# Optimization experiments

Measured on AMD Instinct MI355X. Metric: run time of the kernel, lower is better.

## Reference

```python
import jax, jax.numpy as jnp
import numpy as np

EMBED = 1024
HEADS = 16
HEAD_SIZE = EMBED // HEADS
B, T = 2, 2048
EPS = 1e-5


def layer_norm(x, g, b):
    mu = jnp.mean(x, axis=-1, keepdims=True)
    var = jnp.var(x, axis=-1, keepdims=True)
    return (x - mu) * jax.lax.rsqrt(var + EPS) * g + b


def setup_inputs() -> dict:
    key = jax.random.key(0)
    ks = jax.random.split(key, 12)
    s = 0.02
    return {
        "x": jax.random.normal(ks[0], (B, T, EMBED), jnp.float32),
        "Wq": s * jax.random.normal(ks[1], (EMBED, EMBED), jnp.float32),
        "Wk": s * jax.random.normal(ks[2], (EMBED, EMBED), jnp.float32),
        "Wv": s * jax.random.normal(ks[3], (EMBED, EMBED), jnp.float32),
        "Wo": s * jax.random.normal(ks[4], (EMBED, EMBED), jnp.float32),
        "bo": jnp.zeros((EMBED,), jnp.float32),
        "W1": s * jax.random.normal(ks[5], (EMBED, 4 * EMBED), jnp.float32),
        "b1": jnp.zeros((4 * EMBED,), jnp.float32),
        "W2": s * jax.random.normal(ks[6], (4 * EMBED, EMBED), jnp.float32),
        "b2": jnp.zeros((EMBED,), jnp.float32),
        "ln1_g": jnp.ones((EMBED,), jnp.float32),
        "ln1_b": jnp.zeros((EMBED,), jnp.float32),
        "ln2_g": jnp.ones((EMBED,), jnp.float32),
        "ln2_b": jnp.zeros((EMBED,), jnp.float32),
    }


def reference(x, Wq, Wk, Wv, Wo, bo, W1, b1, W2, b2, ln1_g, ln1_b, ln2_g, ln2_b):
    # --- multi-head causal self-attention on ln1(x) ---
    h = layer_norm(x, ln1_g, ln1_b)                      # [B,T,D]
    q = (h @ Wq).reshape(B, T, HEADS, HEAD_SIZE)         # per-head Q (concat layout)
    k = (h @ Wk).reshape(B, T, HEADS, HEAD_SIZE)
    v = (h @ Wv).reshape(B, T, HEADS, HEAD_SIZE)
    scores = jnp.einsum("bqhd,bkhd->bhqk", q, k) / jnp.sqrt(
        jnp.asarray(HEAD_SIZE, x.dtype)
    )                                                    # [B,H,T,T]
    causal = jnp.tril(jnp.ones((T, T), bool))
    scores = jnp.where(causal, scores, -jnp.inf)
    wei = jax.nn.softmax(scores, axis=-1)
    attn = jnp.einsum("bhqk,bkhd->bqhd", wei, v).reshape(B, T, EMBED)
    x = x + attn @ Wo + bo                               # residual (dropout=0)
    # --- feed-forward on ln2(x) ---
    h2 = layer_norm(x, ln2_g, ln2_b)
    ff = jax.nn.relu(h2 @ W1 + b1) @ W2 + b2
    return x + ff
```

## Files before the change

kernel.cpp:

```cpp
#include <hip/hip_runtime.h>


typedef __bf16 bf16;
typedef __attribute__((ext_vector_type(8))) __bf16 bf16x8;
typedef __attribute__((ext_vector_type(4))) __bf16 bf16x4;
typedef __attribute__((ext_vector_type(4))) short  shortx4;
typedef __attribute__((ext_vector_type(4))) float  floatx4;

__device__ __forceinline__ short f2bf_bits(float x) {
  return __builtin_bit_cast(short, (bf16)x);
}

__device__ __forceinline__ void gl2lds16(const bf16* g, bf16* l) {
  __builtin_amdgcn_global_load_lds((const __attribute__((address_space(1))) void*)g,
                                   (__attribute__((address_space(3))) void*)l, 16, 0, 0);
}

__global__ __launch_bounds__(256) void transpose_cvt(
    const float* __restrict__ Wq, const float* __restrict__ Wk,
    const float* __restrict__ Wv, const float* __restrict__ Wo,
    const float* __restrict__ W1, const float* __restrict__ W2,
    bf16* __restrict__ WqkvT, bf16* __restrict__ WoT,
    bf16* __restrict__ W1T, bf16* __restrict__ W2T)
{
  int id = blockIdx.x;
  const float* src; bf16* dst; int K, N, tile;
  if (id < 4096) {
    K = 1024; N = 1024; tile = id & 1023;
    int wsel = id >> 10;
    src = (wsel == 0) ? Wq : (wsel == 1) ? Wk : (wsel == 2) ? Wv : Wo;
    dst = (wsel < 3) ? (WqkvT + (size_t)wsel * 1024 * 1024) : WoT;
  } else if (id < 8192) {
    K = 1024; N = 4096; tile = id - 4096; src = W1; dst = W1T;
  } else {
    K = 4096; N = 1024; tile = id - 8192; src = W2; dst = W2T;
  }
  int ntn = N >> 5;
  int k0 = (tile / ntn) * 32, n0 = (tile % ntn) * 32;
  __shared__ float tl[32][33];
  int tr = threadIdx.x >> 3, tc = (threadIdx.x & 7) * 4;
  float4 v = *(const float4*)(src + (size_t)(k0 + tr) * N + n0 + tc);
  tl[tr][tc + 0] = v.x; tl[tr][tc + 1] = v.y; tl[tr][tc + 2] = v.z; tl[tr][tc + 3] = v.w;
  __syncthreads();
  bf16x4 o = { (bf16)tl[tc + 0][tr], (bf16)tl[tc + 1][tr],
               (bf16)tl[tc + 2][tr], (bf16)tl[tc + 3][tr] };
  *(bf16x4*)(dst + (size_t)(n0 + tr) * K + k0 + tc) = o;
}

__global__ __launch_bounds__(256) void ln_kernel(
    const float* __restrict__ x, const float* __restrict__ gam,
    const float* __restrict__ bet, bf16* __restrict__ out)
{
  const int row = blockIdx.x, t = threadIdx.x;
  const float* xr = x + (size_t)row * 1024;
  float4 v = *(const float4*)(xr + t * 4);
  float s  = v.x + v.y + v.z + v.w;
  float s2 = v.x * v.x + v.y * v.y + v.z * v.z + v.w * v.w;
  #pragma unroll
  for (int off = 1; off < 64; off <<= 1) {
    s  += __shfl_xor(s, off);
    s2 += __shfl_xor(s2, off);
  }
  __shared__ float ps[4], ps2[4];
  int wv = t >> 6;
  if ((t & 63) == 0) { ps[wv] = s; ps2[wv] = s2; }
  __syncthreads();
  s  = ps[0] + ps[1] + ps[2] + ps[3];
  s2 = ps2[0] + ps2[1] + ps2[2] + ps2[3];
  const float mu = s * (1.0f / 1024.0f);
  const float rstd = rsqrtf(s2 * (1.0f / 1024.0f) - mu * mu + 1e-5f);
  float4 gv = *(const float4*)(gam + t * 4);
  float4 bv = *(const float4*)(bet + t * 4);
  bf16x4 o;
  o[0] = (bf16)((v.x - mu) * rstd * gv.x + bv.x);
  o[1] = (bf16)((v.y - mu) * rstd * gv.y + bv.y);
  o[2] = (bf16)((v.z - mu) * rstd * gv.z + bv.z);
  o[3] = (bf16)((v.w - mu) * rstd * gv.w + bv.w);
  *(bf16x4*)(out + (size_t)row * 1024 + t * 4) = o;
}

template<bool BIAS, bool RELU, bool RESID>
__global__ __launch_bounds__(256) void gemm_kernel(
    const bf16* __restrict__ A, const bf16* __restrict__ Bt,
    const float* __restrict__ bias, const float* __restrict__ resid,
    bf16* __restrict__ Cb, float* __restrict__ Cf,
    int M, int N, int K)
{
  __shared__ bf16 As[128 * 32];
  __shared__ bf16 Bs[128 * 32];
  const int tid = threadIdx.x, lane = tid & 63, wv = tid >> 6;
  const int li = lane & 15, g = lane >> 4;
  const int m0 = blockIdx.x * 128, n0 = blockIdx.y * 128;
  const int wm = wv >> 1, wn = wv & 1;
  const int srow = wv * 16 + (lane >> 2);
  const int scol = (lane & 3) * 8;
  const bf16* aP = A  + (size_t)(m0 + srow) * K + scol;
  const bf16* bP = Bt + (size_t)(n0 + srow) * K + scol;
  bf16* AsW = As + wv * 512;
  bf16* BsW = Bs + wv * 512;
  floatx4 acc[4][4] = {};
  for (int kt = 0; kt < K; kt += 32) {
    gl2lds16(aP + kt,                    AsW);
    gl2lds16(aP + kt + (size_t)64 * K,   AsW + 2048);
    gl2lds16(bP + kt,                    BsW);
    gl2lds16(bP + kt + (size_t)64 * K,   BsW + 2048);
    __syncthreads();
    bf16x8 af[4], bfr[4];
    #pragma unroll
    for (int r = 0; r < 4; ++r)
      af[r] = *(const bf16x8*)(As + (wm * 64 + r * 16 + li) * 32 + g * 8);
    #pragma unroll
    for (int c = 0; c < 4; ++c)
      bfr[c] = *(const bf16x8*)(Bs + (wn * 64 + c * 16 + li) * 32 + g * 8);
    #pragma unroll
    for (int r = 0; r < 4; ++r)
      #pragma unroll
      for (int c = 0; c < 4; ++c)
        acc[r][c] = __builtin_amdgcn_mfma_f32_16x16x32_bf16(af[r], bfr[c], acc[r][c], 0, 0, 0);
    __syncthreads();
  }
  #pragma unroll
  for (int r = 0; r < 4; ++r) {
    int row = m0 + wm * 64 + r * 16 + g * 4;
    #pragma unroll
    for (int c = 0; c < 4; ++c) {
      int col = n0 + wn * 64 + c * 16 + li;
      float bv = BIAS ? bias[col] : 0.0f;
      #pragma unroll
      for (int e = 0; e < 4; ++e) {
        float v = acc[r][c][e] + bv;
        if (RELU) v = fmaxf(v, 0.0f);
        size_t idx = (size_t)(row + e) * N + col;
        if (RESID) Cf[idx] = v + resid[idx];
        else       Cb[idx] = (bf16)v;
      }
    }
  }
}

__global__ __launch_bounds__(256) void gemm_splitk(
    const bf16* __restrict__ A, const bf16* __restrict__ Bt,
    bf16* __restrict__ Cp, int M, int N, int Ktot, int Kc)
{
  __shared__ bf16 As[128 * 32];
  __shared__ bf16 Bs[128 * 32];
  const int tid = threadIdx.x, lane = tid & 63, wv = tid >> 6;
  const int li = lane & 15, g = lane >> 4;
  const int m0 = blockIdx.x * 128, n0 = blockIdx.y * 128;
  const int z = blockIdx.z;
  const int wm = wv >> 1, wn = wv & 1;
  const int srow = wv * 16 + (lane >> 2);
  const int scol = (lane & 3) * 8;
  const bf16* aP = A  + (size_t)(m0 + srow) * Ktot + scol;
  const bf16* bP = Bt + (size_t)(n0 + srow) * Ktot + scol;
  bf16* AsW = As + wv * 512;
  bf16* BsW = Bs + wv * 512;
  floatx4 acc[4][4] = {};
  const int k0 = z * Kc;
  for (int kt = k0; kt < k0 + Kc; kt += 32) {
    gl2lds16(aP + kt,                      AsW);
    gl2lds16(aP + kt + (size_t)64 * Ktot,  AsW + 2048);
    gl2lds16(bP + kt,                      BsW);
    gl2lds16(bP + kt + (size_t)64 * Ktot,  BsW + 2048);
    __syncthreads();
    bf16x8 af[4], bfr[4];
    #pragma unroll
    for (int r = 0; r < 4; ++r)
      af[r] = *(const bf16x8*)(As + (wm * 64 + r * 16 + li) * 32 + g * 8);
    #pragma unroll
    for (int c = 0; c < 4; ++c)
      bfr[c] = *(const bf16x8*)(Bs + (wn * 64 + c * 16 + li) * 32 + g * 8);
    #pragma unroll
    for (int r = 0; r < 4; ++r)
      #pragma unroll
      for (int c = 0; c < 4; ++c)
        acc[r][c] = __builtin_amdgcn_mfma_f32_16x16x32_bf16(af[r], bfr[c], acc[r][c], 0, 0, 0);
    __syncthreads();
  }
  bf16* C = Cp + (size_t)z * M * N;
  #pragma unroll
  for (int r = 0; r < 4; ++r) {
    int row = m0 + wm * 64 + r * 16 + g * 4;
    #pragma unroll
    for (int c = 0; c < 4; ++c) {
      int col = n0 + wn * 64 + c * 16 + li;
      #pragma unroll
      for (int e = 0; e < 4; ++e)
        C[(size_t)(row + e) * N + col] = (bf16)acc[r][c][e];
    }
  }
}

__global__ __launch_bounds__(256) void combine_wo_ln2(
    const bf16* __restrict__ P, const float* __restrict__ bo,
    const float* __restrict__ x, const float* __restrict__ gam,
    const float* __restrict__ bet, float* __restrict__ x2, bf16* __restrict__ h2)
{
  const int row = blockIdx.x, t = threadIdx.x;
  const size_t base = (size_t)row * 1024 + t * 4;
  float4 v = *(const float4*)(x + base);
  bf16x4 p0 = *(const bf16x4*)(P + base);
  bf16x4 p1 = *(const bf16x4*)(P + 4194304 + base);
  float4 bv = *(const float4*)(bo + t * 4);
  v.x += (float)p0[0] + (float)p1[0] + bv.x;
  v.y += (float)p0[1] + (float)p1[1] + bv.y;
  v.z += (float)p0[2] + (float)p1[2] + bv.z;
  v.w += (float)p0[3] + (float)p1[3] + bv.w;
  *(float4*)(x2 + base) = v;
  float s  = v.x + v.y + v.z + v.w;
  float s2 = v.x * v.x + v.y * v.y + v.z * v.z + v.w * v.w;
  #pragma unroll
  for (int off = 1; off < 64; off <<= 1) {
    s  += __shfl_xor(s, off);
    s2 += __shfl_xor(s2, off);
  }
  __shared__ float ps[4], ps2[4];
  int wv = t >> 6;
  if ((t & 63) == 0) { ps[wv] = s; ps2[wv] = s2; }
  __syncthreads();
  s  = ps[0] + ps[1] + ps[2] + ps[3];
  s2 = ps2[0] + ps2[1] + ps2[2] + ps2[3];
  const float mu = s * (1.0f / 1024.0f);
  const float rstd = rsqrtf(s2 * (1.0f / 1024.0f) - mu * mu + 1e-5f);
  float4 gv = *(const float4*)(gam + t * 4);
  float4 bb = *(const float4*)(bet + t * 4);
  bf16x4 o;
  o[0] = (bf16)((v.x - mu) * rstd * gv.x + bb.x);
  o[1] = (bf16)((v.y - mu) * rstd * gv.y + bb.y);
  o[2] = (bf16)((v.z - mu) * rstd * gv.z + bb.z);
  o[3] = (bf16)((v.w - mu) * rstd * gv.w + bb.w);
  *(bf16x4*)(h2 + base) = o;
}

__global__ __launch_bounds__(256) void combine_ffn2(
    const bf16* __restrict__ P, const float* __restrict__ b2,
    const float* __restrict__ x2, float* __restrict__ out)
{
  const size_t i = ((size_t)blockIdx.x * 256 + threadIdx.x) * 4;
  const int col = (int)(i & 1023);
  float4 acc = *(const float4*)(x2 + i);
  float4 bv = *(const float4*)(b2 + col);
  acc.x += bv.x; acc.y += bv.y; acc.z += bv.z; acc.w += bv.w;
  #pragma unroll
  for (int z = 0; z < 4; ++z) {
    bf16x4 p = *(const bf16x4*)(P + (size_t)z * 4194304 + i);
    acc.x += (float)p[0]; acc.y += (float)p[1];
    acc.z += (float)p[2]; acc.w += (float)p[3];
  }
  *(float4*)(out + i) = acc;
}

__global__ __launch_bounds__(256, 2) void attn_kernel(
    const bf16* __restrict__ qkv, bf16* __restrict__ attnb)
{
  __shared__ bf16 Ks[64 * 72];
  __shared__ bf16 Vt[64 * 72];
  const int t = threadIdx.x, lane = t & 63, wv = t >> 6;
  const int li = lane & 15, g = lane >> 4;
  const int p = blockIdx.x & 15, h = (blockIdx.x >> 4) & 15, b = blockIdx.x >> 8;
  const int row0 = b << 11;
  const int tlo = p * 4 + wv, thi = 127 - tlo;
  const int q0l = tlo << 4, q0h = thi << 4;
  const size_t qkvbase = (size_t)row0 * 3072 + (size_t)h * 64;

  const bf16* qpl = qkv + qkvbase + (size_t)(q0l + li) * 3072 + g * 8;
  const bf16* qph = qkv + qkvbase + (size_t)(q0h + li) * 3072 + g * 8;
  bf16x8 bl0 = *(const bf16x8*)(qpl), bl1 = *(const bf16x8*)(qpl + 32);
  bf16x8 bh0 = *(const bf16x8*)(qph), bh1 = *(const bf16x8*)(qph + 32);

  floatx4 ol[4] = {}, oh[4] = {};
  float ll = 0.f, lh = 0.f;
  const int cmax = 31 - p;

  auto proc = [&](const bf16x8& bq0, const bf16x8& bq1, float& l_i,
                  floatx4 (&o)[4], int qg, int k0, bool diag) {
    floatx4 sv[4];
    #pragma unroll
    for (int s = 0; s < 4; ++s) {
      const bf16* kr = Ks + (s * 16 + li) * 72 + g * 8;
      bf16x8 a0 = *(const bf16x8*)(kr);
      bf16x8 a1 = *(const bf16x8*)(kr + 32);
      floatx4 z = {0.f, 0.f, 0.f, 0.f};
      z = __builtin_amdgcn_mfma_f32_16x16x32_bf16(a0, bq0, z, 0, 0, 0);
      z = __builtin_amdgcn_mfma_f32_16x16x32_bf16(a1, bq1, z, 0, 0, 0);
      sv[s] = z;
    }
    float pv[4][4];
    float rs = 0.f;
    #pragma unroll
    for (int s = 0; s < 4; ++s)
      #pragma unroll
      for (int e = 0; e < 4; ++e) {
        float val = __expf(sv[s][e] * 0.125f - 4.0f);
        if (diag) {
          int kg = k0 + s * 16 + g * 4 + e;
          val = (kg <= qg) ? val : 0.0f;
        }
        pv[s][e] = val;
        rs += val;
      }
    rs += __shfl_xor(rs, 16);
    rs += __shfl_xor(rs, 32);
    l_i += rs;
    #pragma unroll
    for (int s = 0; s < 4; ++s) {
      shortx4 bp = { f2bf_bits(pv[s][0]), f2bf_bits(pv[s][1]),
                     f2bf_bits(pv[s][2]), f2bf_bits(pv[s][3]) };
      #pragma unroll
      for (int c = 0; c < 4; ++c) {
        shortx4 av = *(const shortx4*)(Vt + (c * 16 + li) * 72 + s * 16 + g * 4);
        o[c] = __builtin_amdgcn_mfma_f32_16x16x16bf16_1k(av, bp, o[c], 0, 0, 0);
      }
    }
  };

  for (int c = 0; c <= cmax; ++c) {
    {
      const size_t kb = qkvbase + (size_t)(c * 64) * 3072 + 1024;
      #pragma unroll
      for (int r = 0; r < 2; ++r) {
        int row = r * 32 + (t >> 3), dc = (t & 7) * 8;
        bf16x8 kvv = *(const bf16x8*)(qkv + kb + (size_t)row * 3072 + dc);
        *(bf16x8*)(Ks + row * 72 + dc) = kvv;
      }
      int key = t >> 2, d0 = (t & 3) * 16;
      const bf16* vs = qkv + qkvbase + (size_t)(c * 64 + key) * 3072 + 2048 + d0;
      bf16x8 v0 = *(const bf16x8*)(vs);
      bf16x8 v1 = *(const bf16x8*)(vs + 8);
      #pragma unroll
      for (int j = 0; j < 8; ++j) {
        Vt[(d0 + j) * 72 + key]     = v0[j];
        Vt[(d0 + 8 + j) * 72 + key] = v1[j];
      }
    }
    __syncthreads();
    proc(bh0, bh1, lh, oh, q0h + li, c * 64, c == cmax);
    if (c <= p) proc(bl0, bl1, ll, ol, q0l + li, c * 64, c == p);
    __syncthreads();
  }

  const float invh = 1.0f / lh, invl = 1.0f / ll;
  #pragma unroll
  for (int c = 0; c < 4; ++c) {
    bf16x4 ovh = { (bf16)(oh[c][0] * invh), (bf16)(oh[c][1] * invh),
                   (bf16)(oh[c][2] * invh), (bf16)(oh[c][3] * invh) };
    *(bf16x4*)(attnb + (size_t)(row0 + q0h + li) * 1024 + h * 64 + c * 16 + g * 4) = ovh;
    bf16x4 ovl = { (bf16)(ol[c][0] * invl), (bf16)(ol[c][1] * invl),
                   (bf16)(ol[c][2] * invl), (bf16)(ol[c][3] * invl) };
    *(bf16x4*)(attnb + (size_t)(row0 + q0l + li) * 1024 + h * 64 + c * 16 + g * 4) = ovl;
  }
}

extern "C" void kernel_launch(void* const* d_in, const int* in_sizes, int n_in,
                              void* d_out, int out_size, void* d_ws, size_t ws_size,
                              hipStream_t stream) {
  (void)in_sizes; (void)n_in; (void)out_size; (void)ws_size;
  const float* x    = (const float*)d_in[0];
  const float* Wq   = (const float*)d_in[1];
  const float* Wk   = (const float*)d_in[2];
  const float* Wv   = (const float*)d_in[3];
  const float* Wo   = (const float*)d_in[4];
  const float* bo   = (const float*)d_in[5];
  const float* W1   = (const float*)d_in[6];
  const float* b1   = (const float*)d_in[7];
  const float* W2   = (const float*)d_in[8];
  const float* b2   = (const float*)d_in[9];
  const float* ln1g = (const float*)d_in[10];
  const float* ln1b = (const float*)d_in[11];
  const float* ln2g = (const float*)d_in[12];
  const float* ln2b = (const float*)d_in[13];
  float* out = (float*)d_out;
  char* ws = (char*)d_ws;

  constexpr size_t OFF_WQKVT = 0;
  constexpr size_t OFF_WOT   = OFF_WQKVT + 3072ull * 1024 * 2;
  constexpr size_t OFF_W1T   = OFF_WOT   + 1024ull * 1024 * 2;
  constexpr size_t OFF_W2T   = OFF_W1T   + 4096ull * 1024 * 2;
  constexpr size_t OFF_H1    = OFF_W2T   + 1024ull * 4096 * 2;
  constexpr size_t OFF_QKV   = OFF_H1    + 4096ull * 1024 * 2;
  constexpr size_t OFF_ATT   = OFF_QKV   + 4096ull * 3072 * 2;
  constexpr size_t OFF_X2    = OFF_ATT   + 4096ull * 1024 * 2;
  constexpr size_t OFF_H2    = OFF_X2    + 4096ull * 1024 * 4;
  constexpr size_t OFF_F1    = OFF_H2    + 4096ull * 1024 * 2;
  constexpr size_t OFF_PART  = OFF_F1    + 4096ull * 4096 * 2;

  bf16*  WqkvT = (bf16*)(ws + OFF_WQKVT);
  bf16*  WoT   = (bf16*)(ws + OFF_WOT);
  bf16*  W1T   = (bf16*)(ws + OFF_W1T);
  bf16*  W2T   = (bf16*)(ws + OFF_W2T);
  bf16*  h1    = (bf16*)(ws + OFF_H1);
  bf16*  qkv   = (bf16*)(ws + OFF_QKV);
  bf16*  attnb = (bf16*)(ws + OFF_ATT);
  float* x2    = (float*)(ws + OFF_X2);
  bf16*  h2    = (bf16*)(ws + OFF_H2);
  bf16*  f1    = (bf16*)(ws + OFF_F1);
  bf16*  part  = (bf16*)(ws + OFF_PART);

  transpose_cvt<<<12288, 256, 0, stream>>>(Wq, Wk, Wv, Wo, W1, W2, WqkvT, WoT, W1T, W2T);
  ln_kernel<<<4096, 256, 0, stream>>>(x, ln1g, ln1b, h1);
  gemm_kernel<false, false, false><<<dim3(32, 24), 256, 0, stream>>>(
      h1, WqkvT, nullptr, nullptr, qkv, nullptr, 4096, 3072, 1024);
  attn_kernel<<<512, 256, 0, stream>>>(qkv, attnb);
  gemm_splitk<<<dim3(32, 8, 2), 256, 0, stream>>>(attnb, WoT, part, 4096, 1024, 1024, 512);
  combine_wo_ln2<<<4096, 256, 0, stream>>>(part, bo, x, ln2g, ln2b, x2, h2);
  gemm_kernel<true, true, false><<<dim3(32, 32), 256, 0, stream>>>(
      h2, W1T, b1, nullptr, f1, nullptr, 4096, 4096, 1024);
  gemm_splitk<<<dim3(32, 8, 4), 256, 0, stream>>>(f1, W2T, part, 4096, 1024, 4096, 1024);
  combine_ffn2<<<4096, 256, 0, stream>>>(part, b2, x2, out);
}
```

Baseline: 378.0 us.

## Swap MFMA operands for vectorized epilogue stores and emit V pre-transposed

Swaps the A/B operands of the MFMA in all GEMMs so each lane holds four consecutive output columns, which lets the epilogue issue vector bf16x4/float4 stores and loads instead of scalar strided ones. A new QKV GEMM writes Q and K as before but scatters V into a per-(batch, head) transposed global buffer. The attention kernel can then load V^T with contiguous 16-byte reads instead of transposing it through scalar LDS writes on every tile. The cost is an uncoalesced scalar scatter in the V epilogue of the QKV GEMM and an extra workspace buffer.

```diff
diff --git a/kernel.cpp b/kernel.cpp
--- a/kernel.cpp
+++ b/kernel.cpp
@@ -116,23 +116,99 @@
     for (int r = 0; r < 4; ++r)
       #pragma unroll
       for (int c = 0; c < 4; ++c)
-        acc[r][c] = __builtin_amdgcn_mfma_f32_16x16x32_bf16(af[r], bfr[c], acc[r][c], 0, 0, 0);
+        acc[r][c] = __builtin_amdgcn_mfma_f32_16x16x32_bf16(bfr[c], af[r], acc[r][c], 0, 0, 0);
     __syncthreads();
   }
   #pragma unroll
   for (int r = 0; r < 4; ++r) {
-    int row = m0 + wm * 64 + r * 16 + g * 4;
+    int rowC = m0 + wm * 64 + r * 16 + li;
     #pragma unroll
     for (int c = 0; c < 4; ++c) {
-      int col = n0 + wn * 64 + c * 16 + li;
-      float bv = BIAS ? bias[col] : 0.0f;
-      #pragma unroll
-      for (int e = 0; e < 4; ++e) {
-        float v = acc[r][c][e] + bv;
-        if (RELU) v = fmaxf(v, 0.0f);
-        size_t idx = (size_t)(row + e) * N + col;
-        if (RESID) Cf[idx] = v + resid[idx];
-        else       Cb[idx] = (bf16)v;
+      int colC = n0 + wn * 64 + c * 16 + g * 4;
+      float4 bv = BIAS ? *(const float4*)(bias + colC) : float4{0, 0, 0, 0};
+      float v0 = acc[r][c][0] + bv.x, v1 = acc[r][c][1] + bv.y;
+      float v2 = acc[r][c][2] + bv.z, v3 = acc[r][c][3] + bv.w;
+      if (RELU) {
+        v0 = fmaxf(v0, 0.f); v1 = fmaxf(v1, 0.f);
+        v2 = fmaxf(v2, 0.f); v3 = fmaxf(v3, 0.f);
+      }
+      size_t idx = (size_t)rowC * N + colC;
+      if (RESID) {
+        float4 rv = *(const float4*)(resid + idx);
+        float4 ov = { v0 + rv.x, v1 + rv.y, v2 + rv.z, v3 + rv.w };
+        *(float4*)(Cf + idx) = ov;
+      } else {
+        bf16x4 ov = { (bf16)v0, (bf16)v1, (bf16)v2, (bf16)v3 };
+        *(bf16x4*)(Cb + idx) = ov;
+      }
+    }
+  }
+}
+
+__global__ __launch_bounds__(256) void gemm_qkv(
+    const bf16* __restrict__ A, const bf16* __restrict__ Bt,
+    bf16* __restrict__ qkv, bf16* __restrict__ VtG)
+{
+  const int K = 1024;
+  __shared__ bf16 As[128 * 32];
+  __shared__ bf16 Bs[128 * 32];
+  const int tid = threadIdx.x, lane = tid & 63, wv = tid >> 6;
+  const int li = lane & 15, g = lane >> 4;
+  const int m0 = blockIdx.x * 128, n0 = blockIdx.y * 128;
+  const int wm = wv >> 1, wn = wv & 1;
+  const int srow = wv * 16 + (lane >> 2);
+  const int scol = (lane & 3) * 8;
+  const bf16* aP = A  + (size_t)(m0 + srow) * K + scol;
+  const bf16* bP = Bt + (size_t)(n0 + srow) * K + scol;
+  bf16* AsW = As + wv * 512;
+  bf16* BsW = Bs + wv * 512;
+  floatx4 acc[4][4] = {};
+  for (int kt = 0; kt < K; kt += 32) {
+    gl2lds16(aP + kt,                    AsW);
+    gl2lds16(aP + kt + (size_t)64 * K,   AsW + 2048);
+    gl2lds16(bP + kt,                    BsW);
+    gl2lds16(bP + kt + (size_t)64 * K,   BsW + 2048);
+    __syncthreads();
+    bf16x8 af[4], bfr[4];
+    #pragma unroll
+    for (int r = 0; r < 4; ++r)
+      af[r] = *(const bf16x8*)(As + (wm * 64 + r * 16 + li) * 32 + g * 8);
+    #pragma unroll
+    for (int c = 0; c < 4; ++c)
+      bfr[c] = *(const bf16x8*)(Bs + (wn * 64 + c * 16 + li) * 32 + g * 8);
+    #pragma unroll
+    for (int r = 0; r < 4; ++r)
+      #pragma unroll
+      for (int c = 0; c < 4; ++c)
+        acc[r][c] = __builtin_amdgcn_mfma_f32_16x16x32_bf16(bfr[c], af[r], acc[r][c], 0, 0, 0);
+    __syncthreads();
+  }
+  if (n0 < 2048) {
+    #pragma unroll
+    for (int r = 0; r < 4; ++r) {
+      int rowC = m0 + wm * 64 + r * 16 + li;
+      #pragma unroll
+      for (int c = 0; c < 4; ++c) {
+        int colC = n0 + wn * 64 + c * 16 + g * 4;
+        bf16x4 ov = { (bf16)acc[r][c][0], (bf16)acc[r][c][1],
+                      (bf16)acc[r][c][2], (bf16)acc[r][c][3] };
+        *(bf16x4*)(qkv + (size_t)rowC * 3072 + colC) = ov;
+      }
+    }
+  } else {
+    #pragma unroll
+    for (int r = 0; r < 4; ++r) {
+      int rowC = m0 + wm * 64 + r * 16 + li;
+      int key = rowC & 2047, bq = rowC >> 11;
+      #pragma unroll
+      for (int c = 0; c < 4; ++c) {
+        int vcol0 = n0 + wn * 64 + c * 16 + g * 4 - 2048;
+        #pragma unroll
+        for (int e = 0; e < 4; ++e) {
+          int vcol = vcol0 + e;
+          int hh = vcol >> 6, d = vcol & 63;
+          VtG[((size_t)(bq * 16 + hh) * 64 + d) * 2048 + key] = (bf16)acc[r][c][e];
+        }
       }
     }
   }
@@ -174,19 +250,19 @@
     for (int r = 0; r < 4; ++r)
       #pragma unroll
       for (int c = 0; c < 4; ++c)
-        acc[r][c] = __builtin_amdgcn_mfma_f32_16x16x32_bf16(af[r], bfr[c], acc[r][c], 0, 0, 0);
+        acc[r][c] = __builtin_amdgcn_mfma_f32_16x16x32_bf16(bfr[c], af[r], acc[r][c], 0, 0, 0);
     __syncthreads();
   }
   bf16* C = Cp + (size_t)z * M * N;
   #pragma unroll
   for (int r = 0; r < 4; ++r) {
-    int row = m0 + wm * 64 + r * 16 + g * 4;
+    int rowC = m0 + wm * 64 + r * 16 + li;
     #pragma unroll
     for (int c = 0; c < 4; ++c) {
-      int col = n0 + wn * 64 + c * 16 + li;
-      #pragma unroll
-      for (int e = 0; e < 4; ++e)
-        C[(size_t)(row + e) * N + col] = (bf16)acc[r][c][e];
+      int colC = n0 + wn * 64 + c * 16 + g * 4;
+      bf16x4 ov = { (bf16)acc[r][c][0], (bf16)acc[r][c][1],
+                    (bf16)acc[r][c][2], (bf16)acc[r][c][3] };
+      *(bf16x4*)(C + (size_t)rowC * N + colC) = ov;
     }
   }
 }
@@ -251,7 +327,8 @@
 }
 
 __global__ __launch_bounds__(256, 2) void attn_kernel(
-    const bf16* __restrict__ qkv, bf16* __restrict__ attnb)
+    const bf16* __restrict__ qkv, const bf16* __restrict__ VtG,
+    bf16* __restrict__ attnb)
 {
   __shared__ bf16 Ks[64 * 72];
   __shared__ bf16 Vt[64 * 72];
@@ -262,6 +339,7 @@
   const int tlo = p * 4 + wv, thi = 127 - tlo;
   const int q0l = tlo << 4, q0h = thi << 4;
   const size_t qkvbase = (size_t)row0 * 3072 + (size_t)h * 64;
+  const bf16* vgbase = VtG + (size_t)(b * 16 + h) * 64 * 2048;
 
   const bf16* qpl = qkv + qkvbase + (size_t)(q0l + li) * 3072 + g * 8;
   const bf16* qph = qkv + qkvbase + (size_t)(q0h + li) * 3072 + g * 8;
@@ -323,15 +401,12 @@
         bf16x8 kvv = *(const bf16x8*)(qkv + kb + (size_t)row * 3072 + dc);
         *(bf16x8*)(Ks + row * 72 + dc) = kvv;
       }
-      int key = t >> 2, d0 = (t & 3) * 16;
-      const bf16* vs = qkv + qkvbase + (size_t)(c * 64 + key) * 3072 + 2048 + d0;
-      bf16x8 v0 = *(const bf16x8*)(vs);
-      bf16x8 v1 = *(const bf16x8*)(vs + 8);
-      #pragma unroll
-      for (int j = 0; j < 8; ++j) {
-        Vt[(d0 + j) * 72 + key]     = v0[j];
-        Vt[(d0 + 8 + j) * 72 + key] = v1[j];
-      }
+      int d = t >> 2, kg = (t & 3) * 16;
+      const bf16* vg = vgbase + (size_t)d * 2048 + c * 64 + kg;
+      bf16x8 v0 = *(const bf16x8*)(vg);
+      bf16x8 v1 = *(const bf16x8*)(vg + 8);
+      *(bf16x8*)(Vt + d * 72 + kg)     = v0;
+      *(bf16x8*)(Vt + d * 72 + kg + 8) = v1;
     }
     __syncthreads();
     proc(bh0, bh1, lh, oh, q0h + li, c * 64, c == cmax);
@@ -383,6 +458,7 @@
   constexpr size_t OFF_H2    = OFF_X2    + 4096ull * 1024 * 4;
   constexpr size_t OFF_F1    = OFF_H2    + 4096ull * 1024 * 2;
   constexpr size_t OFF_PART  = OFF_F1    + 4096ull * 4096 * 2;
+  constexpr size_t OFF_VTG   = OFF_PART  + 4ull * 4096 * 1024 * 2;
 
   bf16*  WqkvT = (bf16*)(ws + OFF_WQKVT);
   bf16*  WoT   = (bf16*)(ws + OFF_WOT);
@@ -395,12 +471,12 @@
   bf16*  h2    = (bf16*)(ws + OFF_H2);
   bf16*  f1    = (bf16*)(ws + OFF_F1);
   bf16*  part  = (bf16*)(ws + OFF_PART);
+  bf16*  vtg   = (bf16*)(ws + OFF_VTG);
 
   transpose_cvt<<<12288, 256, 0, stream>>>(Wq, Wk, Wv, Wo, W1, W2, WqkvT, WoT, W1T, W2T);
   ln_kernel<<<4096, 256, 0, stream>>>(x, ln1g, ln1b, h1);
-  gemm_kernel<false, false, false><<<dim3(32, 24), 256, 0, stream>>>(
-      h1, WqkvT, nullptr, nullptr, qkv, nullptr, 4096, 3072, 1024);
-  attn_kernel<<<512, 256, 0, stream>>>(qkv, attnb);
+  gemm_qkv<<<dim3(32, 24), 256, 0, stream>>>(h1, WqkvT, qkv, vtg);
+  attn_kernel<<<512, 256, 0, stream>>>(qkv, vtg, attnb);
   gemm_splitk<<<dim3(32, 8, 2), 256, 0, stream>>>(attnb, WoT, part, 4096, 1024, 1024, 512);
   combine_wo_ln2<<<4096, 256, 0, stream>>>(part, bo, x, ln2g, ln2b, x2, h2);
   gemm_kernel<true, true, false><<<dim3(32, 32), 256, 0, stream>>>(
```

Measured after the change: 380.4 us. Within noise of the previous version (+0.6%).
